# Optimization experiments

Hardware: AMD Instinct MI355X
Metric: run time of the kernel (lower is better)

Reference implementation:

```python
import jax, jax.numpy as jnp
import numpy as np

D = 8  # polynomial degree; with bias present, basis has D columns (P1..PD)


def setup_inputs() -> dict:
    key = jax.random.key(0)
    k1, k2 = jax.random.split(key)
    batch, n_in, n_out = 65536, 256, 64
    x = jax.random.normal(k1, (batch, n_in), dtype=jnp.float32)
    c_basis = jax.random.normal(k2, (n_out, n_in, D), dtype=jnp.float32) * (1.0 / np.sqrt(n_in * D))
    bias = jnp.zeros((n_out,), dtype=jnp.float32)
    return {"x": x, "c_basis": c_basis, "bias": bias}


def _legendre_basis(x):
    # x: (batch, n_in). Returns (batch, n_in, D) = [P1(t), ..., PD(t)], t = tanh(x).
    t = jnp.tanh(x)
    p_prev = jnp.ones_like(t)  # P0
    p_curr = t                 # P1
    polys = [p_curr]
    for k in range(2, D + 1):  # small fixed-length loop over degree
        p_next = ((2 * k - 1) * t * p_curr - (k - 1) * p_prev) / k
        polys.append(p_next)
        p_prev, p_curr = p_curr, p_next
    return jnp.stack(polys, axis=-1)  # (batch, n_in, D)


def reference(x, c_basis, bias):
    # basis: (batch, n_in, D); contract over (n_in, D) with c_basis (n_out, n_in, D)
    leg = _legendre_basis(x)
    y = jnp.einsum('bid,oid->bo', leg, c_basis)
    return y + bias
```

## Files before the change

kernel.cpp:

```cpp
#include <hip/hip_runtime.h>
#include <hip/hip_bf16.h>

typedef __attribute__((ext_vector_type(8))) short short8;
typedef __attribute__((ext_vector_type(4))) float floatx4;
typedef __attribute__((ext_vector_type(4))) unsigned int uintx4;

#define GLOBAL_AS __attribute__((address_space(1)))
#define LDS_AS __attribute__((address_space(3)))

__device__ __forceinline__ void async_ld16(const void* g, void* l) {
  __builtin_amdgcn_global_load_lds((const GLOBAL_AS unsigned int*)g,
                                   (LDS_AS unsigned int*)l, 16, 0, 0);
}

__device__ __forceinline__ unsigned pack2_bf16(float a, float b) {
  __hip_bfloat162 h = __float22bfloat162_rn(make_float2(a, b));
  unsigned r;
  __builtin_memcpy(&r, &h, 4);
  return r;
}

__device__ __forceinline__ short8 legendre_frag(float xv) {
  float e  = __builtin_amdgcn_exp2f(xv * 2.885390081777927f);
  float t  = 1.0f - 2.0f * __builtin_amdgcn_rcpf(e + 1.0f);
  float p1 = t;
  float p2 = fmaf(1.5f * t, p1, -0.5f);
  float p3 = fmaf((5.0f / 3.0f) * t, p2, (-2.0f / 3.0f) * p1);
  float p4 = fmaf(1.75f * t, p3, -0.75f * p2);
  float p5 = fmaf(1.8f * t, p4, -0.8f * p3);
  float p6 = fmaf((11.0f / 6.0f) * t, p5, (-5.0f / 6.0f) * p4);
  float p7 = fmaf((13.0f / 7.0f) * t, p6, (-6.0f / 7.0f) * p5);
  float p8 = fmaf(1.875f * t, p7, -0.875f * p6);
  union { unsigned u[4]; short8 s; } r;
  r.u[0] = pack2_bf16(p1, p2);
  r.u[1] = pack2_bf16(p3, p4);
  r.u[2] = pack2_bf16(p5, p6);
  r.u[3] = pack2_bf16(p7, p8);
  return r.s;
}

__global__ void conv_kernel(const float* __restrict__ cb, unsigned short* __restrict__ ws) {
  int t = blockIdx.x * 256 + threadIdx.x;
  int o = t >> 8;
  int i = t & 255;
  const floatx4* s = (const floatx4*)(cb + ((size_t)o * 256 + i) * 8);
  floatx4 v0 = s[0], v1 = s[1];
  uintx4 w;
  w.x = pack2_bf16(v0.x, v0.y);
  w.y = pack2_bf16(v0.z, v0.w);
  w.z = pack2_bf16(v1.x, v1.y);
  w.w = pack2_bf16(v1.z, v1.w);
  *(uintx4*)(ws + (size_t)(i >> 5) * 16384 + (i & 31) * 512 + o * 8) = w;
}

#define MB 64
#define NCH 8

__global__ __launch_bounds__(128, 2) void kan_kernel(
    const float* __restrict__ x, const unsigned short* __restrict__ ws,
    const float* __restrict__ bias, float* __restrict__ y) {
  __shared__ __align__(16) float xs[MB * 32];
  __shared__ __align__(16) unsigned short bt[32 * 64 * 8];

  const int tid  = threadIdx.x;
  const int wid  = tid >> 6;
  const int lane = tid & 63;
  const int m    = lane & 15;
  const int q    = lane >> 4;
  const int row_block = blockIdx.x * MB;

  floatx4 acc[2][4];
#pragma unroll
  for (int a = 0; a < 2; ++a)
#pragma unroll
    for (int nt = 0; nt < 4; ++nt) acc[a][nt] = (floatx4){0.f, 0.f, 0.f, 0.f};

  const int r0 = wid * 32 + m;
  const int xb0 = r0 * 128 + ((m & 7) << 4) + q * 4;
  const int xb1 = xb0 + 16 * 128;
  const unsigned short* btbase = &bt[(q * 64 + m) * 8];

  const float* xsrc[4];
#pragma unroll
  for (int t = 0; t < 4; ++t) {
    int slot = (wid * 4 + t) * 64 + lane;
    int rr   = slot >> 3;
    int si4  = (slot & 7) ^ (rr & 7);
    xsrc[t] = x + (size_t)(row_block + rr) * 256 + si4 * 4;
  }
  const unsigned short* bsrc = ws + (size_t)(wid * 64 + lane) * 8;

  for (int ch = 0; ch < NCH; ++ch) {
    __syncthreads();

#pragma unroll
    for (int t = 0; t < 4; ++t) {
      int slot_base = (wid * 4 + t) * 64;
      async_ld16(xsrc[t], &xs[slot_base * 4]);
      xsrc[t] += 32;
    }
#pragma unroll
    for (int t = 0; t < 16; ++t) {
      int slot_base = t * 128 + wid * 64;
      async_ld16(bsrc + (size_t)ch * 16384 + (size_t)t * 1024, &bt[slot_base * 8]);
    }
    __syncthreads();

#pragma unroll
    for (int ks = 0; ks < 8; ++ks) {
      short8 fb[4];
#pragma unroll
      for (int nt = 0; nt < 4; ++nt) {
        fb[nt] = *(const short8*)(btbase + ks * 2048 + nt * 128);
      }
      float xv0 = *(const float*)((const char*)xs + (xb0 ^ (ks << 4)));
      float xv1 = *(const float*)((const char*)xs + (xb1 ^ (ks << 4)));
      short8 fa0 = legendre_frag(xv0);
      short8 fa1 = legendre_frag(xv1);
#pragma unroll
      for (int nt = 0; nt < 4; ++nt) {
        acc[0][nt] = __builtin_amdgcn_mfma_f32_16x16x32_bf16(fa0, fb[nt], acc[0][nt], 0, 0, 0);
        acc[1][nt] = __builtin_amdgcn_mfma_f32_16x16x32_bf16(fa1, fb[nt], acc[1][nt], 0, 0, 0);
      }
    }
  }

  float bv[4];
#pragma unroll
  for (int nt = 0; nt < 4; ++nt) bv[nt] = bias[nt * 16 + m];
#pragma unroll
  for (int a = 0; a < 2; ++a) {
    int gr0 = row_block + wid * 32 + a * 16 + q * 4;
#pragma unroll
    for (int nt = 0; nt < 4; ++nt) {
#pragma unroll
      for (int r = 0; r < 4; ++r) {
        y[(size_t)(gr0 + r) * 64 + nt * 16 + m] = acc[a][nt][r] + bv[nt];
      }
    }
  }
}

extern "C" void kernel_launch(void* const* d_in, const int* in_sizes, int n_in,
                              void* d_out, int out_size, void* d_ws, size_t ws_size,
                              hipStream_t stream) {
  const float* x    = (const float*)d_in[0];
  const float* cb   = (const float*)d_in[1];
  const float* bias = (const float*)d_in[2];
  float* y = (float*)d_out;
  unsigned short* ws = (unsigned short*)d_ws;
  int batch = in_sizes[0] / 256;
  hipLaunchKernelGGL(conv_kernel, dim3(64), dim3(256), 0, stream, cb, ws);
  hipLaunchKernelGGL(kan_kernel, dim3(batch / MB), dim3(128), 0, stream, x, ws, bias, y);
}
```

Baseline: 127.7 us.

## Drop LDS staging; load x and weights directly from global with register prefetch

Removes the shared-memory tiles and barriers. Each lane now reads its x values and bf16 weight fragments straight from global memory, prefetching the next step into registers, and the weight layout is simplified to match. The Legendre recurrence is rewritten with cheaper FMAs, and a truncating-style bf16 pack via perm replaces the round-to-nearest conversion for activations. The aim is to cut barrier and LDS overhead and per-element ALU work. In exchange, x loads become scattered 4-byte reads across rows, with no coalescing, and the weight reuse now goes through cache instead of LDS.

Result: slower. 139.8 us (+9.5%).

```diff
diff --git a/kernel.cpp b/kernel.cpp
--- a/kernel.cpp
+++ b/kernel.cpp
@@ -5,69 +5,62 @@
 typedef __attribute__((ext_vector_type(4))) float floatx4;
 typedef __attribute__((ext_vector_type(4))) unsigned int uintx4;
 
-#define GLOBAL_AS __attribute__((address_space(1)))
-#define LDS_AS __attribute__((address_space(3)))
-
-__device__ __forceinline__ void async_ld16(const void* g, void* l) {
-  __builtin_amdgcn_global_load_lds((const GLOBAL_AS unsigned int*)g,
-                                   (LDS_AS unsigned int*)l, 16, 0, 0);
-}
-
-__device__ __forceinline__ unsigned pack2_bf16(float a, float b) {
+__device__ __forceinline__ unsigned pack2_bf16_rn(float a, float b) {
   __hip_bfloat162 h = __float22bfloat162_rn(make_float2(a, b));
   unsigned r;
   __builtin_memcpy(&r, &h, 4);
   return r;
 }
 
+__device__ __forceinline__ unsigned pack2_bf16_fast(float a, float b) {
+  unsigned ua, ub;
+  __builtin_memcpy(&ua, &a, 4);
+  __builtin_memcpy(&ub, &b, 4);
+  return __builtin_amdgcn_perm(ub + 0x8000u, ua + 0x8000u, 0x07060302u);
+}
+
 __device__ __forceinline__ short8 legendre_frag(float xv) {
   float e  = __builtin_amdgcn_exp2f(xv * 2.885390081777927f);
   float t  = 1.0f - 2.0f * __builtin_amdgcn_rcpf(e + 1.0f);
   float p1 = t;
-  float p2 = fmaf(1.5f * t, p1, -0.5f);
-  float p3 = fmaf((5.0f / 3.0f) * t, p2, (-2.0f / 3.0f) * p1);
-  float p4 = fmaf(1.75f * t, p3, -0.75f * p2);
-  float p5 = fmaf(1.8f * t, p4, -0.8f * p3);
-  float p6 = fmaf((11.0f / 6.0f) * t, p5, (-5.0f / 6.0f) * p4);
-  float p7 = fmaf((13.0f / 7.0f) * t, p6, (-6.0f / 7.0f) * p5);
-  float p8 = fmaf(1.875f * t, p7, -0.875f * p6);
+  float u2 = t * p1,  w2 = u2 - 1.0f;        float p2 = fmaf(0.5f, w2, u2);
+  float u3 = t * p2,  w3 = u3 - p1;          float p3 = fmaf(2.0f/3.0f, w3, u3);
+  float u4 = t * p3,  w4 = u4 - p2;          float p4 = fmaf(0.75f, w4, u4);
+  float u5 = t * p4,  w5 = u5 - p3;          float p5 = fmaf(0.8f, w5, u5);
+  float u6 = t * p5,  w6 = u6 - p4;          float p6 = fmaf(5.0f/6.0f, w6, u6);
+  float u7 = t * p6,  w7 = u7 - p5;          float p7 = fmaf(6.0f/7.0f, w7, u7);
+  float u8 = t * p7,  w8 = u8 - p6;          float p8 = fmaf(7.0f/8.0f, w8, u8);
   union { unsigned u[4]; short8 s; } r;
-  r.u[0] = pack2_bf16(p1, p2);
-  r.u[1] = pack2_bf16(p3, p4);
-  r.u[2] = pack2_bf16(p5, p6);
-  r.u[3] = pack2_bf16(p7, p8);
+  r.u[0] = pack2_bf16_fast(p1, p2);
+  r.u[1] = pack2_bf16_fast(p3, p4);
+  r.u[2] = pack2_bf16_fast(p5, p6);
+  r.u[3] = pack2_bf16_fast(p7, p8);
   return r.s;
 }
 
 __global__ void conv_kernel(const float* __restrict__ cb, unsigned short* __restrict__ ws) {
   int t = blockIdx.x * 256 + threadIdx.x;
-  int o = t >> 8;
-  int i = t & 255;
+  int o = t & 63;
+  int i = t >> 6;
   const floatx4* s = (const floatx4*)(cb + ((size_t)o * 256 + i) * 8);
   floatx4 v0 = s[0], v1 = s[1];
   uintx4 w;
-  w.x = pack2_bf16(v0.x, v0.y);
-  w.y = pack2_bf16(v0.z, v0.w);
-  w.z = pack2_bf16(v1.x, v1.y);
-  w.w = pack2_bf16(v1.z, v1.w);
-  *(uintx4*)(ws + (size_t)(i >> 5) * 16384 + (i & 31) * 512 + o * 8) = w;
+  w.x = pack2_bf16_rn(v0.x, v0.y);
+  w.y = pack2_bf16_rn(v0.z, v0.w);
+  w.z = pack2_bf16_rn(v1.x, v1.y);
+  w.w = pack2_bf16_rn(v1.z, v1.w);
+  *(uintx4*)(ws + (size_t)i * 512 + o * 8) = w;
 }
-
-#define MB 64
-#define NCH 8
 
 __global__ __launch_bounds__(128, 2) void kan_kernel(
     const float* __restrict__ x, const unsigned short* __restrict__ ws,
     const float* __restrict__ bias, float* __restrict__ y) {
-  __shared__ __align__(16) float xs[MB * 32];
-  __shared__ __align__(16) unsigned short bt[32 * 64 * 8];
-
   const int tid  = threadIdx.x;
   const int wid  = tid >> 6;
   const int lane = tid & 63;
   const int m    = lane & 15;
   const int q    = lane >> 4;
-  const int row_block = blockIdx.x * MB;
+  const int row_block = blockIdx.x * 64;
 
   floatx4 acc[2][4];
 #pragma unroll
@@ -75,54 +68,38 @@
 #pragma unroll
     for (int nt = 0; nt < 4; ++nt) acc[a][nt] = (floatx4){0.f, 0.f, 0.f, 0.f};
 
-  const int r0 = wid * 32 + m;
-  const int xb0 = r0 * 128 + ((m & 7) << 4) + q * 4;
-  const int xb1 = xb0 + 16 * 128;
-  const unsigned short* btbase = &bt[(q * 64 + m) * 8];
+  const int r0g = row_block + wid * 32 + m;
+  const float* xp0 = x + (size_t)r0g * 256 + q;
+  const float* xp1 = xp0 + 16 * 256;
+  const unsigned short* bp = ws + q * 512 + m * 8;
 
-  const float* xsrc[4];
+  short8 fbN[4];
 #pragma unroll
-  for (int t = 0; t < 4; ++t) {
-    int slot = (wid * 4 + t) * 64 + lane;
-    int rr   = slot >> 3;
-    int si4  = (slot & 7) ^ (rr & 7);
-    xsrc[t] = x + (size_t)(row_block + rr) * 256 + si4 * 4;
-  }
-  const unsigned short* bsrc = ws + (size_t)(wid * 64 + lane) * 8;
+  for (int nt = 0; nt < 4; ++nt) fbN[nt] = *(const short8*)(bp + nt * 128);
+  float xvN0 = xp0[0];
+  float xvN1 = xp1[0];
 
-  for (int ch = 0; ch < NCH; ++ch) {
-    __syncthreads();
+#pragma unroll 2
+  for (int s = 0; s < 64; ++s) {
+    short8 fb0 = fbN[0], fb1 = fbN[1], fb2 = fbN[2], fb3 = fbN[3];
+    float xv0 = xvN0, xv1 = xvN1;
+    int sn = (s < 63) ? (s + 1) : 63;
+#pragma unroll
+    for (int nt = 0; nt < 4; ++nt)
+      fbN[nt] = *(const short8*)(bp + (size_t)sn * 2048 + nt * 128);
+    xvN0 = xp0[sn * 4];
+    xvN1 = xp1[sn * 4];
 
-#pragma unroll
-    for (int t = 0; t < 4; ++t) {
-      int slot_base = (wid * 4 + t) * 64;
-      async_ld16(xsrc[t], &xs[slot_base * 4]);
-      xsrc[t] += 32;
-    }
-#pragma unroll
-    for (int t = 0; t < 16; ++t) {
-      int slot_base = t * 128 + wid * 64;
-      async_ld16(bsrc + (size_t)ch * 16384 + (size_t)t * 1024, &bt[slot_base * 8]);
-    }
-    __syncthreads();
-
-#pragma unroll
-    for (int ks = 0; ks < 8; ++ks) {
-      short8 fb[4];
-#pragma unroll
-      for (int nt = 0; nt < 4; ++nt) {
-        fb[nt] = *(const short8*)(btbase + ks * 2048 + nt * 128);
-      }
-      float xv0 = *(const float*)((const char*)xs + (xb0 ^ (ks << 4)));
-      float xv1 = *(const float*)((const char*)xs + (xb1 ^ (ks << 4)));
-      short8 fa0 = legendre_frag(xv0);
-      short8 fa1 = legendre_frag(xv1);
-#pragma unroll
-      for (int nt = 0; nt < 4; ++nt) {
-        acc[0][nt] = __builtin_amdgcn_mfma_f32_16x16x32_bf16(fa0, fb[nt], acc[0][nt], 0, 0, 0);
-        acc[1][nt] = __builtin_amdgcn_mfma_f32_16x16x32_bf16(fa1, fb[nt], acc[1][nt], 0, 0, 0);
-      }
-    }
+    short8 fa0 = legendre_frag(xv0);
+    short8 fa1 = legendre_frag(xv1);
+    acc[0][0] = __builtin_amdgcn_mfma_f32_16x16x32_bf16(fa0, fb0, acc[0][0], 0, 0, 0);
+    acc[1][0] = __builtin_amdgcn_mfma_f32_16x16x32_bf16(fa1, fb0, acc[1][0], 0, 0, 0);
+    acc[0][1] = __builtin_amdgcn_mfma_f32_16x16x32_bf16(fa0, fb1, acc[0][1], 0, 0, 0);
+    acc[1][1] = __builtin_amdgcn_mfma_f32_16x16x32_bf16(fa1, fb1, acc[1][1], 0, 0, 0);
+    acc[0][2] = __builtin_amdgcn_mfma_f32_16x16x32_bf16(fa0, fb2, acc[0][2], 0, 0, 0);
+    acc[1][2] = __builtin_amdgcn_mfma_f32_16x16x32_bf16(fa1, fb2, acc[1][2], 0, 0, 0);
+    acc[0][3] = __builtin_amdgcn_mfma_f32_16x16x32_bf16(fa0, fb3, acc[0][3], 0, 0, 0);
+    acc[1][3] = __builtin_amdgcn_mfma_f32_16x16x32_bf16(fa1, fb3, acc[1][3], 0, 0, 0);
   }
 
   float bv[4];
@@ -151,5 +128,5 @@
   unsigned short* ws = (unsigned short*)d_ws;
   int batch = in_sizes[0] / 256;
   hipLaunchKernelGGL(conv_kernel, dim3(64), dim3(256), 0, stream, cb, ws);
-  hipLaunchKernelGGL(kan_kernel, dim3(batch / MB), dim3(128), 0, stream, x, ws, bias, y);
+  hipLaunchKernelGGL(kan_kernel, dim3(batch / 64), dim3(128), 0, stream, x, ws, bias, y);
 }
```
